# Optimization experiments

Hardware: AMD Instinct MI355X
Metric: run time of the kernel (lower is better)

The kernel has to match this reference:

```python
import jax, jax.numpy as jnp
import numpy as np

N, E, DIN, DH, DOUT, G, H = 40000, 400000, 256, 128, 128, 256, 4
BN_EPS = 1e-5      # nn.BatchNorm1d default
SM_EPS = 1e-16     # PyG softmax eps
NEG_SLOPE = 0.2    # GATConv default negative_slope


def _gat(x, src, dst, W, a_src, a_dst, b, heads, out_ch):
    # x:[N,Fin] W:[Fin,heads*out_ch] a_*:[heads,out_ch] b:[out_ch]
    n = x.shape[0]
    h = (x @ W).reshape(n, heads, out_ch)                     # [N,H,C]
    e = (h * a_src).sum(-1)[src] + (h * a_dst).sum(-1)[dst]   # [E,H] attention logits
    e = jnp.where(e > 0, e, NEG_SLOPE * e)                    # leaky_relu
    m = jax.ops.segment_max(e, dst, num_segments=n)           # segment softmax over incoming edges
    p = jnp.exp(e - m[dst])
    z = jax.ops.segment_sum(p, dst, num_segments=n)
    alpha = p / (z[dst] + SM_EPS)                             # [E,H]
    out = jax.ops.segment_sum(h[src] * alpha[:, :, None], dst, num_segments=n)  # [N,H,C]
    return out.mean(axis=1) + b                               # concat=False -> mean over heads, then bias


def _bn(x, g, b, m, v):
    # eval-mode BatchNorm1d with running stats
    return (x - m) * jax.lax.rsqrt(v + BN_EPS) * g + b


def setup_inputs():
    key = jax.random.key(0)
    ks = jax.random.split(key, 16)
    def rn(k, shape, fan):
        return jax.random.normal(k, shape, jnp.float32) / np.sqrt(fan).astype(np.float32)
    return {
        "x": jax.random.normal(ks[0], (N, DIN), jnp.float32),
        "src": jax.random.randint(ks[1], (E,), 0, N),
        "dst": jax.random.randint(ks[2], (E,), 0, N),
        "batch": jnp.sort(jax.random.randint(ks[3], (N,), 0, G)),
        "W1": rn(ks[4], (DIN, H * DH), DIN), "as1": rn(ks[5], (H, DH), DH), "ad1": rn(ks[6], (H, DH), DH), "b1": jnp.zeros((DH,), jnp.float32),
        "g1": jnp.ones((DH,), jnp.float32), "be1": jnp.zeros((DH,), jnp.float32), "m1": jnp.zeros((DH,), jnp.float32), "v1": jnp.ones((DH,), jnp.float32),
        "W2": rn(ks[7], (DH, H * DH), DH), "as2": rn(ks[8], (H, DH), DH), "ad2": rn(ks[9], (H, DH), DH), "b2": jnp.zeros((DH,), jnp.float32),
        "g2": jnp.ones((DH,), jnp.float32), "be2": jnp.zeros((DH,), jnp.float32), "m2": jnp.zeros((DH,), jnp.float32), "v2": jnp.ones((DH,), jnp.float32),
        "W3": rn(ks[10], (DH, DOUT), DH), "as3": rn(ks[11], (1, DOUT), DOUT), "ad3": rn(ks[12], (1, DOUT), DOUT), "b3": jnp.zeros((DOUT,), jnp.float32),
    }


def reference(x, src, dst, batch, W1, as1, ad1, b1, g1, be1, m1, v1,
              W2, as2, ad2, b2, g2, be2, m2, v2, W3, as3, ad3, b3):
    n = x.shape[0]
    loop = jnp.arange(n)
    s = jnp.concatenate([src, loop])  # PyG GATConv add_self_loops=True
    d = jnp.concatenate([dst, loop])
    h = jax.nn.elu(_gat(x, s, d, W1, as1, ad1, b1, H, DH))
    h = _bn(h, g1, be1, m1, v1)
    h = jax.nn.elu(_gat(h, s, d, W2, as2, ad2, b2, H, DH))
    h = _bn(h, g2, be2, m2, v2)
    h = _gat(h, s, d, W3, as3, ad3, b3, 1, DOUT)
    tot = jax.ops.segment_sum(h, batch, num_segments=G)      # global_mean_pool
    cnt = jax.ops.segment_sum(jnp.ones((n,), h.dtype), batch, num_segments=G)
    return tot / jnp.maximum(cnt, 1.0)[:, None]
```

## Files before the change

kernel.cpp:

```cpp
#include <hip/hip_runtime.h>
#include <cstdint>

#define N_NODES 40000
#define N_EDGES 400000
#define DIN 256
#define DHID 128
#define NG 256
#define NHEAD 4
#define ETOT (N_EDGES + N_NODES)

typedef __attribute__((ext_vector_type(8))) short short8;
typedef __attribute__((ext_vector_type(8))) unsigned short bfx8;
typedef __attribute__((ext_vector_type(4))) unsigned short bfx4;
typedef __attribute__((ext_vector_type(4))) float floatx4;

static __device__ __forceinline__ unsigned short f2bf(float f) {
    unsigned u = __float_as_uint(f);
    unsigned r = (u + 0x7FFFu + ((u >> 16) & 1u)) >> 16;
    return (unsigned short)r;
}
static __device__ __forceinline__ float bf2f(unsigned short s) {
    return __uint_as_float((unsigned)s << 16);
}


#define NB_CNT 1719
#define NB_W1  512
#define NB_W2  256
#define NB_W3  64

__global__ void prep_kernel(const int* __restrict__ dst, int* __restrict__ deg,
                            const float* __restrict__ W1, unsigned short* __restrict__ W1t,
                            const float* __restrict__ W2, unsigned short* __restrict__ W2t,
                            const float* __restrict__ W3, unsigned short* __restrict__ W3t) {
    int b = blockIdx.x;
    if (b < NB_CNT) {
        int i = b * 256 + threadIdx.x;
        if (i >= ETOT) return;
        int d = (i < N_EDGES) ? dst[i] : (i - N_EDGES);
        atomicAdd(&deg[d], 1);
    } else if (b < NB_CNT + NB_W1) {
        int i = (b - NB_CNT) * 256 + threadIdx.x;
        int k = i >> 9, n = i & 511;
        W1t[(size_t)n * 256 + k] = f2bf(W1[i]);
    } else if (b < NB_CNT + NB_W1 + NB_W2) {
        int i = (b - NB_CNT - NB_W1) * 256 + threadIdx.x;
        int k = i >> 9, n = i & 511;
        W2t[(size_t)n * 128 + k] = f2bf(W2[i]);
    } else {
        int i = (b - NB_CNT - NB_W1 - NB_W2) * 256 + threadIdx.x;
        int k = i >> 7, n = i & 127;
        W3t[(size_t)n * 128 + k] = f2bf(W3[i]);
    }
}


__global__ __launch_bounds__(1024) void scan_kernel(const int* __restrict__ deg,
                                                    int* __restrict__ offs,
                                                    int* __restrict__ cursor) {
    const int IT = 40;
    __shared__ int wsum[16];
    int t = threadIdx.x;
    int lane = t & 63, wv = t >> 6;
    int base = wv * 2560;
    int vals[IT];
    int lsum = 0;
#pragma unroll
    for (int i = 0; i < IT; i++) {
        int idx = base + i * 64 + lane;
        int v = (idx < N_NODES) ? deg[idx] : 0;
        vals[i] = v;
        lsum += v;
    }
#pragma unroll
    for (int m = 32; m >= 1; m >>= 1) lsum += __shfl_xor(lsum, m, 64);
    if (lane == 0) wsum[wv] = lsum;
    __syncthreads();
    if (t == 0) {
        int c = 0;
#pragma unroll
        for (int i = 0; i < 16; i++) { int v = wsum[i]; wsum[i] = c; c += v; }
    }
    __syncthreads();
    int carry = wsum[wv];
#pragma unroll
    for (int i = 0; i < IT; i++) {
        int v = vals[i];
        int inc = v;
#pragma unroll
        for (int off = 1; off < 64; off <<= 1) {
            int n = __shfl_up(inc, off, 64);
            if (lane >= off) inc += n;
        }
        int tot = __shfl(inc, 63, 64);
        int idx = base + i * 64 + lane;
        if (idx < N_NODES) { int o = carry + inc - v; offs[idx] = o; cursor[idx] = o; }
        carry += tot;
    }
    if (t == 0) offs[N_NODES] = ETOT;
}

__global__ void fill_kernel(const int* __restrict__ src, const int* __restrict__ dst,
                            int* __restrict__ cursor, int* __restrict__ csr) {
    int i = blockIdx.x * 256 + threadIdx.x;
    if (i >= ETOT) return;
    int s, d;
    if (i < N_EDGES) { s = src[i]; d = dst[i]; } else { s = d = i - N_EDGES; }
    int pos = atomicAdd(&cursor[d], 1);
    csr[pos] = s;
}


template <int K, int SH, bool AF32>
__global__ __launch_bounds__(256) void mfma_gemm_kernel(const void* __restrict__ Aptr,
                                                        const unsigned short* __restrict__ Bt,
                                                        unsigned short* __restrict__ C,
                                                        const float* __restrict__ asrc,
                                                        const float* __restrict__ adst,
                                                        float* __restrict__ ssrc,
                                                        float* __restrict__ sdst) {
    constexpr int KC = 128;
    constexpr int KP = KC + 8;
    constexpr int NCOL = SH * 128;
    __shared__ alignas(16) unsigned short A_lds[64][KP];
    __shared__ alignas(16) unsigned short B_lds[128][KP];

    const int tid = threadIdx.x;
    const int lane = tid & 63, wave = tid >> 6;
    const int row0 = blockIdx.x * 64;
    const int cq = lane & 15, rq = lane >> 4;

    floatx4 acc[SH][4][2] = {};

    for (int k0 = 0; k0 < K; k0 += KC) {
        __syncthreads();
#pragma unroll
        for (int r = 0; r < 4; r++) {
            int i = r * 256 + tid;
            int row = i >> 4, slot = i & 15;
            if constexpr (AF32) {
                const float* ap = (const float*)Aptr + (size_t)(row0 + row) * K + k0 + slot * 8;
                float4 u0 = *(const float4*)ap;
                float4 u1 = *(const float4*)(ap + 4);
                short8 v;
                v[0] = (short)f2bf(u0.x); v[1] = (short)f2bf(u0.y);
                v[2] = (short)f2bf(u0.z); v[3] = (short)f2bf(u0.w);
                v[4] = (short)f2bf(u1.x); v[5] = (short)f2bf(u1.y);
                v[6] = (short)f2bf(u1.z); v[7] = (short)f2bf(u1.w);
                *(short8*)&A_lds[row][slot * 8] = v;
            } else {
                const unsigned short* ap = (const unsigned short*)Aptr + (size_t)(row0 + row) * K + k0 + slot * 8;
                *(short8*)&A_lds[row][slot * 8] = *(const short8*)ap;
            }
        }
#pragma unroll
        for (int h = 0; h < SH; h++) {
            if (h) __syncthreads();
#pragma unroll
            for (int r = 0; r < 8; r++) {
                int i = r * 256 + tid;
                int col = i >> 4, slot = i & 15;
                short8 v = *(const short8*)(Bt + (size_t)(h * 128 + col) * K + k0 + slot * 8);
                *(short8*)&B_lds[col][slot * 8] = v;
            }
            __syncthreads();
#pragma unroll
            for (int kk = 0; kk < KC; kk += 32) {
                short8 af[4], bfr[2];
#pragma unroll
                for (int i = 0; i < 4; i++)
                    af[i] = *(const short8*)&A_lds[i * 16 + cq][kk + rq * 8];
#pragma unroll
                for (int j = 0; j < 2; j++)
                    bfr[j] = *(const short8*)&B_lds[wave * 32 + j * 16 + cq][kk + rq * 8];
#pragma unroll
                for (int i = 0; i < 4; i++)
#pragma unroll
                    for (int j = 0; j < 2; j++)
                        acc[h][i][j] = __builtin_amdgcn_mfma_f32_16x16x32_bf16(af[i], bfr[j], acc[h][i][j], 0, 0, 0);
            }
        }
    }

#pragma unroll
    for (int h = 0; h < SH; h++)
#pragma unroll
        for (int i = 0; i < 4; i++)
#pragma unroll
            for (int j = 0; j < 2; j++) {
                unsigned short* cp = C + (size_t)(row0 + i * 16 + rq * 4) * NCOL + h * 128 + wave * 32 + j * 16 + cq;
#pragma unroll
                for (int r = 0; r < 4; r++)
                    cp[(size_t)r * NCOL] = f2bf(acc[h][i][j][r]);
            }

    float* sred = (float*)&A_lds[0][0];
    float* dred = sred + 256;
#pragma unroll
    for (int h = 0; h < SH; h++) {
        const float* ah = asrc + h * 128;
        const float* dh = adst + h * 128;
        float a0 = ah[wave * 32 + cq], a1 = ah[wave * 32 + 16 + cq];
        float d0 = dh[wave * 32 + cq], d1 = dh[wave * 32 + 16 + cq];
        __syncthreads();
#pragma unroll
        for (int i = 0; i < 4; i++)
#pragma unroll
            for (int r = 0; r < 4; r++) {
                float ss = acc[h][i][0][r] * a0 + acc[h][i][1][r] * a1;
                float sd = acc[h][i][0][r] * d0 + acc[h][i][1][r] * d1;
#pragma unroll
                for (int m = 1; m <= 8; m <<= 1) {
                    ss += __shfl_xor(ss, m, 64);
                    sd += __shfl_xor(sd, m, 64);
                }
                if (cq == 0) {
                    int row = i * 16 + rq * 4 + r;
                    sred[wave * 64 + row] = ss;
                    dred[wave * 64 + row] = sd;
                }
            }
        __syncthreads();
        if (tid < 64) {
            float ss = sred[tid] + sred[64 + tid] + sred[128 + tid] + sred[192 + tid];
            float sd = dred[tid] + dred[64 + tid] + dred[128 + tid] + dred[192 + tid];
            ssrc[(size_t)(row0 + tid) * SH + h] = ss;
            sdst[(size_t)(row0 + tid) * SH + h] = sd;
        }
    }
}


__global__ __launch_bounds__(256) void agg4_kernel(const int* __restrict__ offs,
                                                   const int* __restrict__ csr,
                                                   const unsigned short* __restrict__ hbuf,
                                                   const float4* __restrict__ ssrc4,
                                                   const float4* __restrict__ sdst4,
                                                   const float* __restrict__ bias,
                                                   const float* __restrict__ bng,
                                                   const float* __restrict__ bnb,
                                                   const float* __restrict__ bnm,
                                                   const float* __restrict__ bnv,
                                                   unsigned short* __restrict__ outb) {
    __shared__ alignas(16) float aload[4][64][4];
    __shared__ int sload[4][64];

    int wave = threadIdx.x >> 6, lane = threadIdx.x & 63;
    int d = blockIdx.x * 4 + wave;
    int off = offs[d];
    int deg = offs[d + 1] - off;
    int hh = lane >> 4;
    float4 sdv = sdst4[d];
    float acc[8] = {};

    if (deg <= 64) {
        int sreg = 0;
        float4 ev;
        if (lane < deg) {
            sreg = csr[off + lane];
            float4 es = ssrc4[sreg];
            ev.x = es.x + sdv.x; ev.x = ev.x > 0.f ? ev.x : 0.2f * ev.x;
            ev.y = es.y + sdv.y; ev.y = ev.y > 0.f ? ev.y : 0.2f * ev.y;
            ev.z = es.z + sdv.z; ev.z = ev.z > 0.f ? ev.z : 0.2f * ev.z;
            ev.w = es.w + sdv.w; ev.w = ev.w > 0.f ? ev.w : 0.2f * ev.w;
        } else { ev.x = ev.y = ev.z = ev.w = -1e30f; }
        float4 mx = ev;
#pragma unroll
        for (int m = 32; m >= 1; m >>= 1) {
            mx.x = fmaxf(mx.x, __shfl_xor(mx.x, m, 64));
            mx.y = fmaxf(mx.y, __shfl_xor(mx.y, m, 64));
            mx.z = fmaxf(mx.z, __shfl_xor(mx.z, m, 64));
            mx.w = fmaxf(mx.w, __shfl_xor(mx.w, m, 64));
        }
        float4 p;
        p.x = (lane < deg) ? __expf(ev.x - mx.x) : 0.f;
        p.y = (lane < deg) ? __expf(ev.y - mx.y) : 0.f;
        p.z = (lane < deg) ? __expf(ev.z - mx.z) : 0.f;
        p.w = (lane < deg) ? __expf(ev.w - mx.w) : 0.f;
        float4 z = p;
#pragma unroll
        for (int m = 32; m >= 1; m >>= 1) {
            z.x += __shfl_xor(z.x, m, 64);
            z.y += __shfl_xor(z.y, m, 64);
            z.z += __shfl_xor(z.z, m, 64);
            z.w += __shfl_xor(z.w, m, 64);
        }
        float4 alpha;
        alpha.x = p.x / (z.x + 1e-16f);
        alpha.y = p.y / (z.y + 1e-16f);
        alpha.z = p.z / (z.z + 1e-16f);
        alpha.w = p.w / (z.w + 1e-16f);

        *(float4*)&aload[wave][lane][0] = alpha;
        sload[wave][lane] = sreg;

        int j = 0;
        for (; j + 3 < deg; j += 4) {
            int s0 = sload[wave][j],     s1 = sload[wave][j + 1];
            int s2 = sload[wave][j + 2], s3 = sload[wave][j + 3];
            float a0 = aload[wave][j][hh],     a1 = aload[wave][j + 1][hh];
            float a2 = aload[wave][j + 2][hh], a3 = aload[wave][j + 3][hh];
            bfx8 v0 = *(const bfx8*)(hbuf + (size_t)s0 * 512 + lane * 8);
            bfx8 v1 = *(const bfx8*)(hbuf + (size_t)s1 * 512 + lane * 8);
            bfx8 v2 = *(const bfx8*)(hbuf + (size_t)s2 * 512 + lane * 8);
            bfx8 v3 = *(const bfx8*)(hbuf + (size_t)s3 * 512 + lane * 8);
#pragma unroll
            for (int i = 0; i < 8; i++)
                acc[i] += a0 * bf2f(v0[i]) + a1 * bf2f(v1[i]) +
                          a2 * bf2f(v2[i]) + a3 * bf2f(v3[i]);
        }
        for (; j < deg; j++) {
            int s = sload[wave][j];
            float a = aload[wave][j][hh];
            bfx8 hv = *(const bfx8*)(hbuf + (size_t)s * 512 + lane * 8);
#pragma unroll
            for (int i = 0; i < 8; i++) acc[i] += a * bf2f(hv[i]);
        }
    } else {
        float4 mx; mx.x = mx.y = mx.z = mx.w = -1e30f;
        for (int j = lane; j < deg; j += 64) {
            int s = csr[off + j];
            float4 es = ssrc4[s];
            float4 e;
            e.x = es.x + sdv.x; e.x = e.x > 0.f ? e.x : 0.2f * e.x;
            e.y = es.y + sdv.y; e.y = e.y > 0.f ? e.y : 0.2f * e.y;
            e.z = es.z + sdv.z; e.z = e.z > 0.f ? e.z : 0.2f * e.z;
            e.w = es.w + sdv.w; e.w = e.w > 0.f ? e.w : 0.2f * e.w;
            mx.x = fmaxf(mx.x, e.x); mx.y = fmaxf(mx.y, e.y);
            mx.z = fmaxf(mx.z, e.z); mx.w = fmaxf(mx.w, e.w);
        }
#pragma unroll
        for (int m = 32; m >= 1; m >>= 1) {
            mx.x = fmaxf(mx.x, __shfl_xor(mx.x, m, 64));
            mx.y = fmaxf(mx.y, __shfl_xor(mx.y, m, 64));
            mx.z = fmaxf(mx.z, __shfl_xor(mx.z, m, 64));
            mx.w = fmaxf(mx.w, __shfl_xor(mx.w, m, 64));
        }
        float4 z; z.x = z.y = z.z = z.w = 0.f;
        for (int j = lane; j < deg; j += 64) {
            int s = csr[off + j];
            float4 es = ssrc4[s];
            float4 e;
            e.x = es.x + sdv.x; e.x = e.x > 0.f ? e.x : 0.2f * e.x;
            e.y = es.y + sdv.y; e.y = e.y > 0.f ? e.y : 0.2f * e.y;
            e.z = es.z + sdv.z; e.z = e.z > 0.f ? e.z : 0.2f * e.z;
            e.w = es.w + sdv.w; e.w = e.w > 0.f ? e.w : 0.2f * e.w;
            z.x += __expf(e.x - mx.x); z.y += __expf(e.y - mx.y);
            z.z += __expf(e.z - mx.z); z.w += __expf(e.w - mx.w);
        }
#pragma unroll
        for (int m = 32; m >= 1; m >>= 1) {
            z.x += __shfl_xor(z.x, m, 64);
            z.y += __shfl_xor(z.y, m, 64);
            z.z += __shfl_xor(z.z, m, 64);
            z.w += __shfl_xor(z.w, m, 64);
        }
        float mc = hh == 0 ? mx.x : hh == 1 ? mx.y : hh == 2 ? mx.z : mx.w;
        float zc = hh == 0 ? z.x : hh == 1 ? z.y : hh == 2 ? z.z : z.w;
        float ic = 1.f / (zc + 1e-16f);
        float sdc = hh == 0 ? sdv.x : hh == 1 ? sdv.y : hh == 2 ? sdv.z : sdv.w;
        for (int j = 0; j < deg; j++) {
            int s = csr[off + j];
            float4 es = ssrc4[s];
            float ec = hh == 0 ? es.x : hh == 1 ? es.y : hh == 2 ? es.z : es.w;
            ec += sdc; ec = ec > 0.f ? ec : 0.2f * ec;
            float a = __expf(ec - mc) * ic;
            bfx8 hv = *(const bfx8*)(hbuf + (size_t)s * 512 + lane * 8);
#pragma unroll
            for (int i = 0; i < 8; i++) acc[i] += a * bf2f(hv[i]);
        }
    }

#pragma unroll
    for (int i = 0; i < 8; i++) {
        acc[i] += __shfl_xor(acc[i], 16, 64);
        acc[i] += __shfl_xor(acc[i], 32, 64);
    }
    if (lane < 16) {
        int c0 = lane * 8;
        bfx8 o;
#pragma unroll
        for (int i = 0; i < 8; i++) {
            int c = c0 + i;
            float v = acc[i] * 0.25f + bias[c];
            v = v > 0.f ? v : (__expf(v) - 1.0f);
            float sc = bng[c] * rsqrtf(bnv[c] + 1e-5f);
            v = (v - bnm[c]) * sc + bnb[c];
            o[i] = f2bf(v);
        }
        *(bfx8*)(outb + (size_t)d * 128 + c0) = o;
    }
}


__global__ __launch_bounds__(256) void agg1_kernel(const int* __restrict__ offs,
                                                   const int* __restrict__ csr,
                                                   const unsigned short* __restrict__ hbuf1,
                                                   const float* __restrict__ ssrc1,
                                                   const float* __restrict__ sdst1,
                                                   const float* __restrict__ bias,
                                                   float* __restrict__ h3out) {
    __shared__ float aload[4][64];
    __shared__ int sload[4][64];
    int wave = threadIdx.x >> 6, lane = threadIdx.x & 63;
    int d = blockIdx.x * 4 + wave;
    int off = offs[d];
    int deg = offs[d + 1] - off;
    int half = lane >> 5, li = lane & 31;
    float sdv = sdst1[d];
    float acc[4] = {};

    if (deg <= 64) {
        float ev = -1e30f; int sreg = 0;
        if (lane < deg) {
            sreg = csr[off + lane];
            ev = ssrc1[sreg] + sdv;
            ev = ev > 0.f ? ev : 0.2f * ev;
        }
        float mx = ev;
#pragma unroll
        for (int m = 32; m >= 1; m >>= 1) mx = fmaxf(mx, __shfl_xor(mx, m, 64));
        float p = (lane < deg) ? __expf(ev - mx) : 0.f;
        float z = p;
#pragma unroll
        for (int m = 32; m >= 1; m >>= 1) z += __shfl_xor(z, m, 64);
        aload[wave][lane] = p / (z + 1e-16f);
        sload[wave][lane] = sreg;

        int j = half;
        for (; j + 2 < deg; j += 4) {
            int s0 = sload[wave][j], s1 = sload[wave][j + 2];
            float a0 = aload[wave][j], a1 = aload[wave][j + 2];
            bfx4 v0 = *(const bfx4*)(hbuf1 + (size_t)s0 * 128 + li * 4);
            bfx4 v1 = *(const bfx4*)(hbuf1 + (size_t)s1 * 128 + li * 4);
#pragma unroll
            for (int i = 0; i < 4; i++)
                acc[i] += a0 * bf2f(v0[i]) + a1 * bf2f(v1[i]);
        }
        for (; j < deg; j += 2) {
            int s = sload[wave][j];
            float a = aload[wave][j];
            bfx4 hv = *(const bfx4*)(hbuf1 + (size_t)s * 128 + li * 4);
#pragma unroll
            for (int i = 0; i < 4; i++) acc[i] += a * bf2f(hv[i]);
        }
    } else {
        float mx = -1e30f;
        for (int j = lane; j < deg; j += 64) {
            float e = ssrc1[csr[off + j]] + sdv;
            e = e > 0.f ? e : 0.2f * e;
            mx = fmaxf(mx, e);
        }
#pragma unroll
        for (int m = 32; m >= 1; m >>= 1) mx = fmaxf(mx, __shfl_xor(mx, m, 64));
        float z = 0.f;
        for (int j = lane; j < deg; j += 64) {
            float e = ssrc1[csr[off + j]] + sdv;
            e = e > 0.f ? e : 0.2f * e;
            z += __expf(e - mx);
        }
#pragma unroll
        for (int m = 32; m >= 1; m >>= 1) z += __shfl_xor(z, m, 64);
        float inv = 1.f / (z + 1e-16f);
        for (int j = half; j < deg; j += 2) {
            int s = csr[off + j];
            float e = ssrc1[s] + sdv;
            e = e > 0.f ? e : 0.2f * e;
            float a = __expf(e - mx) * inv;
            bfx4 hv = *(const bfx4*)(hbuf1 + (size_t)s * 128 + li * 4);
#pragma unroll
            for (int i = 0; i < 4; i++) acc[i] += a * bf2f(hv[i]);
        }
    }

#pragma unroll
    for (int i = 0; i < 4; i++) acc[i] += __shfl_xor(acc[i], 32, 64);
    if (lane < 32) {
        float4 o;
        o.x = acc[0] + bias[li * 4];
        o.y = acc[1] + bias[li * 4 + 1];
        o.z = acc[2] + bias[li * 4 + 2];
        o.w = acc[3] + bias[li * 4 + 3];
        *(float4*)(h3out + (size_t)d * 128 + li * 4) = o;
    }
}


__global__ __launch_bounds__(256) void pool_kernel(const float* __restrict__ h3,
                                                   const int* __restrict__ batch,
                                                   float* __restrict__ out) {
    __shared__ float red[256];
    int g = blockIdx.x;
    int t = threadIdx.x;
    int lo = 0, n = N_NODES;
    while (n > 0) { int s = n >> 1; if (batch[lo + s] < g) { lo += s + 1; n -= s + 1; } else n = s; }
    int hi = lo; n = N_NODES - lo;
    while (n > 0) { int s = n >> 1; if (batch[hi + s] < g + 1) { hi += s + 1; n -= s + 1; } else n = s; }
    int c = t & 127;
    float acc = 0.f;
    for (int r = lo + (t >> 7); r < hi; r += 2)
        acc += h3[(size_t)r * 128 + c];
    red[t] = acc;
    __syncthreads();
    if (t < 128)
        out[(size_t)g * 128 + t] = (red[t] + red[t + 128]) / fmaxf((float)(hi - lo), 1.0f);
}


extern "C" void kernel_launch(void* const* d_in, const int* in_sizes, int n_in,
                              void* d_out, int out_size, void* d_ws, size_t ws_size,
                              hipStream_t stream) {
    const float* x    = (const float*)d_in[0];
    const int* src    = (const int*)d_in[1];
    const int* dst    = (const int*)d_in[2];
    const int* batch  = (const int*)d_in[3];
    const float* W1   = (const float*)d_in[4];
    const float* as1  = (const float*)d_in[5];
    const float* ad1  = (const float*)d_in[6];
    const float* b1   = (const float*)d_in[7];
    const float* g1   = (const float*)d_in[8];
    const float* be1  = (const float*)d_in[9];
    const float* m1   = (const float*)d_in[10];
    const float* v1   = (const float*)d_in[11];
    const float* W2   = (const float*)d_in[12];
    const float* as2  = (const float*)d_in[13];
    const float* ad2  = (const float*)d_in[14];
    const float* b2   = (const float*)d_in[15];
    const float* g2   = (const float*)d_in[16];
    const float* be2  = (const float*)d_in[17];
    const float* m2   = (const float*)d_in[18];
    const float* v2   = (const float*)d_in[19];
    const float* W3   = (const float*)d_in[20];
    const float* as3  = (const float*)d_in[21];
    const float* ad3  = (const float*)d_in[22];
    const float* b3   = (const float*)d_in[23];
    float* out = (float*)d_out;

    char* w = (char*)d_ws;
    size_t o = 0;
    auto alloc = [&](size_t bytes) -> void* {
        void* p = w + o;
        o += (bytes + 255) & ~(size_t)255;
        return p;
    };
    int* deg     = (int*)alloc((size_t)N_NODES * 4);
    int* offs    = (int*)alloc((size_t)(N_NODES + 1) * 4);
    int* cursor  = (int*)alloc((size_t)N_NODES * 4);
    int* csr     = (int*)alloc((size_t)ETOT * 4);
    float* ssrc  = (float*)alloc((size_t)N_NODES * NHEAD * 4);
    float* sdst  = (float*)alloc((size_t)N_NODES * NHEAD * 4);
    float* h3out = (float*)alloc((size_t)N_NODES * 128 * 4);
    unsigned short* hbuf = (unsigned short*)alloc((size_t)N_NODES * 512 * 2);
    unsigned short* xbuf = (unsigned short*)alloc((size_t)N_NODES * 128 * 2);
    unsigned short* W1t  = (unsigned short*)alloc((size_t)512 * 256 * 2);
    unsigned short* W2t  = (unsigned short*)alloc((size_t)512 * 128 * 2);
    unsigned short* W3t  = (unsigned short*)alloc((size_t)128 * 128 * 2);

    (void)hipMemsetAsync(deg, 0, (size_t)N_NODES * 4, stream);

    prep_kernel<<<NB_CNT + NB_W1 + NB_W2 + NB_W3, 256, 0, stream>>>(
        dst, deg, W1, W1t, W2, W2t, W3, W3t);
    scan_kernel<<<1, 1024, 0, stream>>>(deg, offs, cursor);
    fill_kernel<<<(ETOT + 255) / 256, 256, 0, stream>>>(src, dst, cursor, csr);

    mfma_gemm_kernel<256, 4, true><<<N_NODES / 64, 256, 0, stream>>>(
        x, W1t, hbuf, as1, ad1, ssrc, sdst);
    agg4_kernel<<<N_NODES / 4, 256, 0, stream>>>(offs, csr, hbuf, (const float4*)ssrc,
                                                 (const float4*)sdst, b1, g1, be1, m1, v1, xbuf);

    mfma_gemm_kernel<128, 4, false><<<N_NODES / 64, 256, 0, stream>>>(
        xbuf, W2t, hbuf, as2, ad2, ssrc, sdst);
    agg4_kernel<<<N_NODES / 4, 256, 0, stream>>>(offs, csr, hbuf, (const float4*)ssrc,
                                                 (const float4*)sdst, b2, g2, be2, m2, v2, xbuf);

    mfma_gemm_kernel<128, 1, false><<<N_NODES / 64, 256, 0, stream>>>(
        xbuf, W3t, hbuf, as3, ad3, ssrc, sdst);
    agg1_kernel<<<N_NODES / 4, 256, 0, stream>>>(offs, csr, hbuf, ssrc, sdst, b3, h3out);

    pool_kernel<<<NG, 256, 0, stream>>>(h3out, batch, out);
}
```

Baseline: 500.8 us.

## Split GEMM heads across grid y-dimension instead of looping inside each block

The MFMA GEMM now assigns one 128-column head per block via blockIdx.y, launching 4x more blocks for the 4-head layers instead of having each block loop over all heads. This cuts per-block accumulator registers (acc drops from SH*8 to 8 floatx4), which should improve occupancy and parallelism on the 625-block grid. The trade-off is that each A tile is reloaded and, in layer 1, reconverted from fp32 once per head, so A global traffic rises up to 4x.

```diff
diff --git a/kernel.cpp b/kernel.cpp
--- a/kernel.cpp
+++ b/kernel.cpp
@@ -111,7 +111,7 @@
 }
 
 
-template <int K, int SH, bool AF32>
+template <int K, int NCOL, bool AF32>
 __global__ __launch_bounds__(256) void mfma_gemm_kernel(const void* __restrict__ Aptr,
                                                         const unsigned short* __restrict__ Bt,
                                                         unsigned short* __restrict__ C,
@@ -121,19 +121,21 @@
                                                         float* __restrict__ sdst) {
     constexpr int KC = 128;
     constexpr int KP = KC + 8;
-    constexpr int NCOL = SH * 128;
+    constexpr int SH = NCOL / 128;
     __shared__ alignas(16) unsigned short A_lds[64][KP];
     __shared__ alignas(16) unsigned short B_lds[128][KP];
 
     const int tid = threadIdx.x;
     const int lane = tid & 63, wave = tid >> 6;
     const int row0 = blockIdx.x * 64;
+    const int head = blockIdx.y;
+    const int col0 = head * 128;
     const int cq = lane & 15, rq = lane >> 4;
 
-    floatx4 acc[SH][4][2] = {};
+    floatx4 acc[4][2] = {};
 
     for (int k0 = 0; k0 < K; k0 += KC) {
-        __syncthreads();
+        if (k0) __syncthreads();
 #pragma unroll
         for (int r = 0; r < 4; r++) {
             int i = r * 256 + tid;
@@ -154,79 +156,73 @@
             }
         }
 #pragma unroll
-        for (int h = 0; h < SH; h++) {
-            if (h) __syncthreads();
-#pragma unroll
-            for (int r = 0; r < 8; r++) {
-                int i = r * 256 + tid;
-                int col = i >> 4, slot = i & 15;
-                short8 v = *(const short8*)(Bt + (size_t)(h * 128 + col) * K + k0 + slot * 8);
-                *(short8*)&B_lds[col][slot * 8] = v;
-            }
-            __syncthreads();
-#pragma unroll
-            for (int kk = 0; kk < KC; kk += 32) {
-                short8 af[4], bfr[2];
-#pragma unroll
-                for (int i = 0; i < 4; i++)
-                    af[i] = *(const short8*)&A_lds[i * 16 + cq][kk + rq * 8];
+        for (int r = 0; r < 8; r++) {
+            int i = r * 256 + tid;
+            int col = i >> 4, slot = i & 15;
+            short8 v = *(const short8*)(Bt + (size_t)(col0 + col) * K + k0 + slot * 8);
+            *(short8*)&B_lds[col][slot * 8] = v;
+        }
+        __syncthreads();
+
+#pragma unroll
+        for (int kk = 0; kk < KC; kk += 32) {
+            short8 af[4], bfr[2];
+#pragma unroll
+            for (int i = 0; i < 4; i++)
+                af[i] = *(const short8*)&A_lds[i * 16 + cq][kk + rq * 8];
+#pragma unroll
+            for (int j = 0; j < 2; j++)
+                bfr[j] = *(const short8*)&B_lds[wave * 32 + j * 16 + cq][kk + rq * 8];
+#pragma unroll
+            for (int i = 0; i < 4; i++)
 #pragma unroll
                 for (int j = 0; j < 2; j++)
-                    bfr[j] = *(const short8*)&B_lds[wave * 32 + j * 16 + cq][kk + rq * 8];
-#pragma unroll
-                for (int i = 0; i < 4; i++)
-#pragma unroll
-                    for (int j = 0; j < 2; j++)
-                        acc[h][i][j] = __builtin_amdgcn_mfma_f32_16x16x32_bf16(af[i], bfr[j], acc[h][i][j], 0, 0, 0);
-            }
-        }
-    }
-
-#pragma unroll
-    for (int h = 0; h < SH; h++)
-#pragma unroll
-        for (int i = 0; i < 4; i++)
-#pragma unroll
-            for (int j = 0; j < 2; j++) {
-                unsigned short* cp = C + (size_t)(row0 + i * 16 + rq * 4) * NCOL + h * 128 + wave * 32 + j * 16 + cq;
-#pragma unroll
-                for (int r = 0; r < 4; r++)
-                    cp[(size_t)r * NCOL] = f2bf(acc[h][i][j][r]);
-            }
-
+                    acc[i][j] = __builtin_amdgcn_mfma_f32_16x16x32_bf16(af[i], bfr[j], acc[i][j], 0, 0, 0);
+        }
+    }
+
+#pragma unroll
+    for (int i = 0; i < 4; i++)
+#pragma unroll
+        for (int j = 0; j < 2; j++) {
+            unsigned short* cp = C + (size_t)(row0 + i * 16 + rq * 4) * NCOL + col0 + wave * 32 + j * 16 + cq;
+#pragma unroll
+            for (int r = 0; r < 4; r++)
+                cp[(size_t)r * NCOL] = f2bf(acc[i][j][r]);
+        }
+
+    const float* ah = asrc + head * 128;
+    const float* dh = adst + head * 128;
+    float a0 = ah[wave * 32 + cq], a1 = ah[wave * 32 + 16 + cq];
+    float d0 = dh[wave * 32 + cq], d1 = dh[wave * 32 + 16 + cq];
+
+    __syncthreads();
     float* sred = (float*)&A_lds[0][0];
     float* dred = sred + 256;
-#pragma unroll
-    for (int h = 0; h < SH; h++) {
-        const float* ah = asrc + h * 128;
-        const float* dh = adst + h * 128;
-        float a0 = ah[wave * 32 + cq], a1 = ah[wave * 32 + 16 + cq];
-        float d0 = dh[wave * 32 + cq], d1 = dh[wave * 32 + 16 + cq];
-        __syncthreads();
-#pragma unroll
-        for (int i = 0; i < 4; i++)
-#pragma unroll
-            for (int r = 0; r < 4; r++) {
-                float ss = acc[h][i][0][r] * a0 + acc[h][i][1][r] * a1;
-                float sd = acc[h][i][0][r] * d0 + acc[h][i][1][r] * d1;
-#pragma unroll
-                for (int m = 1; m <= 8; m <<= 1) {
-                    ss += __shfl_xor(ss, m, 64);
-                    sd += __shfl_xor(sd, m, 64);
-                }
-                if (cq == 0) {
-                    int row = i * 16 + rq * 4 + r;
-                    sred[wave * 64 + row] = ss;
-                    dred[wave * 64 + row] = sd;
-                }
+
+#pragma unroll
+    for (int i = 0; i < 4; i++)
+#pragma unroll
+        for (int r = 0; r < 4; r++) {
+            float ss = acc[i][0][r] * a0 + acc[i][1][r] * a1;
+            float sd = acc[i][0][r] * d0 + acc[i][1][r] * d1;
+#pragma unroll
+            for (int m = 1; m <= 8; m <<= 1) {
+                ss += __shfl_xor(ss, m, 64);
+                sd += __shfl_xor(sd, m, 64);
             }
-        __syncthreads();
-        if (tid < 64) {
-            float ss = sred[tid] + sred[64 + tid] + sred[128 + tid] + sred[192 + tid];
-            float sd = dred[tid] + dred[64 + tid] + dred[128 + tid] + dred[192 + tid];
-            ssrc[(size_t)(row0 + tid) * SH + h] = ss;
-            sdst[(size_t)(row0 + tid) * SH + h] = sd;
-        }
+            if (cq == 0) {
+                int row = i * 16 + rq * 4 + r;
+                sred[wave * 64 + row] = ss;
+                dred[wave * 64 + row] = sd;
+            }
+        }
+    __syncthreads();
+    if (tid < 64) {
+        float ss = sred[tid] + sred[64 + tid] + sred[128 + tid] + sred[192 + tid];
+        float sd = dred[tid] + dred[64 + tid] + dred[128 + tid] + dred[192 + tid];
+        ssrc[(size_t)(row0 + tid) * SH + head] = ss;
+        sdst[(size_t)(row0 + tid) * SH + head] = sd;
     }
 }
 
@@ -563,17 +559,17 @@
     scan_kernel<<<1, 1024, 0, stream>>>(deg, offs, cursor);
     fill_kernel<<<(ETOT + 255) / 256, 256, 0, stream>>>(src, dst, cursor, csr);
 
-    mfma_gemm_kernel<256, 4, true><<<N_NODES / 64, 256, 0, stream>>>(
+    mfma_gemm_kernel<256, 512, true><<<dim3(N_NODES / 64, 4), 256, 0, stream>>>(
         x, W1t, hbuf, as1, ad1, ssrc, sdst);
     agg4_kernel<<<N_NODES / 4, 256, 0, stream>>>(offs, csr, hbuf, (const float4*)ssrc,
                                                  (const float4*)sdst, b1, g1, be1, m1, v1, xbuf);
 
-    mfma_gemm_kernel<128, 4, false><<<N_NODES / 64, 256, 0, stream>>>(
+    mfma_gemm_kernel<128, 512, false><<<dim3(N_NODES / 64, 4), 256, 0, stream>>>(
         xbuf, W2t, hbuf, as2, ad2, ssrc, sdst);
     agg4_kernel<<<N_NODES / 4, 256, 0, stream>>>(offs, csr, hbuf, (const float4*)ssrc,
                                                  (const float4*)sdst, b2, g2, be2, m2, v2, xbuf);
 
-    mfma_gemm_kernel<128, 1, false><<<N_NODES / 64, 256, 0, stream>>>(
+    mfma_gemm_kernel<128, 128, false><<<dim3(N_NODES / 64, 1), 256, 0, stream>>>(
         xbuf, W3t, hbuf, as3, ad3, ssrc, sdst);
     agg1_kernel<<<N_NODES / 4, 256, 0, stream>>>(offs, csr, hbuf, ssrc, sdst, b3, h3out);
 
```

Measured after the change: 435.5 us (median of 2 runs). -13.0%, faster.
